# Optimization experiments

Hardware: AMD Instinct MI355X
Metric: run time of the kernel (lower is better)

Reference implementation:

```python
import jax, jax.numpy as jnp
import numpy as np

DIM = 1024
HEADS = 16
DIM_HEAD = 64
DEPTH = 12
LN_EPS = 1e-5


def setup_inputs() -> dict:
    key = jax.random.key(0)
    k1, k2, k3 = jax.random.split(key, 3)
    B, N = 4, 2048
    inner = HEADS * DIM_HEAD
    x = jax.random.normal(k1, (B, N, DIM), dtype=jnp.float32)
    ln_w = jnp.ones((DIM,), jnp.float32)
    ln_b = jnp.zeros((DIM,), jnp.float32)
    w_qkv = jax.random.normal(k2, (DIM, 3 * inner), jnp.float32) * (DIM ** -0.5)
    w_out = jax.random.normal(k3, (inner, DIM), jnp.float32) * (inner ** -0.5)
    b_out = jnp.zeros((DIM,), jnp.float32)
    return {"x": x, "ln_w": ln_w, "ln_b": ln_b, "w_qkv": w_qkv,
            "w_out": w_out, "b_out": b_out, "layer_index": 2}


def reference(x, ln_w, ln_b, w_qkv, w_out, b_out, layer_index):
    B, N, D = x.shape
    scale = DIM_HEAD ** -0.5
    # LayerNorm
    mu = jnp.mean(x, axis=-1, keepdims=True)
    var = jnp.mean(jnp.square(x - mu), axis=-1, keepdims=True)
    xn = (x - mu) * jax.lax.rsqrt(var + LN_EPS) * ln_w + ln_b
    # QKV projection (no bias), split heads: b n (h d) -> b h n d
    qkv = xn @ w_qkv  # [B, N, 3*H*Dh]
    q, k, v = jnp.split(qkv, 3, axis=-1)
    def heads(t):
        return t.reshape(B, N, HEADS, DIM_HEAD).transpose(0, 2, 1, 3)
    q, k, v = heads(q), heads(k), heads(v)
    dots = jnp.einsum('bhnd,bhmd->bhnm', q, k) * scale  # [B,H,N,N]
    if layer_index < DEPTH // 2:
        attn = jax.nn.relu(dots)
    else:
        attn = jax.nn.softmax(dots, axis=-1)
    attn = attn / N  # divide by x.shape[1]
    out = jnp.einsum('bhnm,bhmd->bhnd', attn, v)
    out = out.transpose(0, 2, 1, 3).reshape(B, N, HEADS * DIM_HEAD)
    # to_out (heads > 1): Linear + (inactive) dropout
    return out @ w_out + b_out
```

## Files before the change

### kernel.cpp

```cpp
#include <hip/hip_runtime.h>
#include <stdint.h>

typedef __bf16 bf16x8 __attribute__((ext_vector_type(8)));
typedef __bf16 bf16x4 __attribute__((ext_vector_type(4)));
typedef short short4s __attribute__((ext_vector_type(4)));
typedef float f32x4 __attribute__((ext_vector_type(4)));

#define PSCALE (0.125f / 2048.0f)

#define GLOAD16(src, dst)                                                      \
  __builtin_amdgcn_global_load_lds(                                            \
      (__attribute__((address_space(1))) void*)const_cast<__bf16*>(src),       \
      (__attribute__((address_space(3))) void*)(dst), 16, 0, 0)

__global__ __launch_bounds__(256) void ln_fused(const float* __restrict__ x,
                                                const float* __restrict__ w,
                                                const float* __restrict__ b,
                                                __bf16* __restrict__ xn) {
  const int row = blockIdx.x;
  const int t = threadIdx.x;
  const float4 v = ((const float4*)(x + (size_t)row * 1024))[t];
  float s = v.x + v.y + v.z + v.w;
  float ss = v.x * v.x + v.y * v.y + v.z * v.z + v.w * v.w;
#pragma unroll
  for (int o = 32; o; o >>= 1) {
    s += __shfl_down(s, o);
    ss += __shfl_down(ss, o);
  }
  __shared__ float red[8];
  if ((t & 63) == 0) {
    red[t >> 6] = s;
    red[4 + (t >> 6)] = ss;
  }
  __syncthreads();
  const float tot = red[0] + red[1] + red[2] + red[3];
  const float tot2 = red[4] + red[5] + red[6] + red[7];
  const float mu = tot * (1.0f / 1024.0f);
  const float var = tot2 * (1.0f / 1024.0f) - mu * mu;
  const float rs = rsqrtf(var + 1e-5f);
  const float4 wv = ((const float4*)w)[t];
  const float4 bv = ((const float4*)b)[t];
  bf16x4 o;
  o[0] = (__bf16)((v.x - mu) * rs * wv.x + bv.x);
  o[1] = (__bf16)((v.y - mu) * rs * wv.y + bv.y);
  o[2] = (__bf16)((v.z - mu) * rs * wv.z + bv.z);
  o[3] = (__bf16)((v.w - mu) * rs * wv.w + bv.w);
  ((bf16x4*)xn)[(size_t)row * 256 + t] = o;
}

__global__ __launch_bounds__(256) void transpose_cvt(const float* __restrict__ A,
                                                     __bf16* __restrict__ At,
                                                     int R, int C) {
  __shared__ __bf16 T[64][72];
  const int rb = blockIdx.y * 64, cb = blockIdx.x * 64;
  const int tid = threadIdx.x;
  const int r = tid >> 2, cg = tid & 3;
#pragma unroll
  for (int k = 0; k < 4; ++k) {
    const float4 v =
        *(const float4*)(A + (size_t)(rb + r) * C + cb + cg * 16 + k * 4);
    T[cg * 16 + k * 4 + 0][r] = (__bf16)v.x;
    T[cg * 16 + k * 4 + 1][r] = (__bf16)v.y;
    T[cg * 16 + k * 4 + 2][r] = (__bf16)v.z;
    T[cg * 16 + k * 4 + 3][r] = (__bf16)v.w;
  }
  __syncthreads();
#pragma unroll
  for (int i = 0; i < 2; ++i) {
    const int j = i * 256 + tid;
    const int c = j >> 3, s8 = j & 7;
    const bf16x8 o = *(const bf16x8*)&T[c][s8 * 8];
    *(bf16x8*)(At + (size_t)(cb + c) * R + rb + s8 * 8) = o;
  }
}

__device__ __forceinline__ void stage_128x64(const __bf16* __restrict__ g,
                                             int ld, __bf16* lds) {
  const int lane = threadIdx.x & 63, w = threadIdx.x >> 6;
#pragma unroll
  for (int i = 0; i < 4; ++i) {
    const int j = i * 256 + w * 64 + lane;
    const int row = j >> 3, slot = j & 7;
    const __bf16* src = g + (size_t)row * ld + ((slot ^ (row & 7)) << 3);
    GLOAD16(src, lds + (size_t)(i * 256 + w * 64) * 8);
  }
}

__device__ __forceinline__ void stage_vt(const __bf16* __restrict__ g,
                                         __bf16* lds) {
  const int lane = threadIdx.x & 63, w = threadIdx.x >> 6;
#pragma unroll
  for (int i = 0; i < 4; ++i) {
    const int j = i * 256 + w * 64 + lane;
    const int d = j >> 4, slot = j & 15;
    const __bf16* src = g + (size_t)d * 2048 + ((slot ^ (d & 7)) << 3);
    GLOAD16(src, lds + (size_t)(i * 256 + w * 64) * 8);
  }
}

template <int MODE>
__global__ __launch_bounds__(256) void gemm_nt(
    const __bf16* __restrict__ A, const __bf16* __restrict__ B, int K,
    float* __restrict__ outF, __bf16* __restrict__ Qo, __bf16* __restrict__ Ko,
    __bf16* __restrict__ Vto, const float* __restrict__ bias) {
  __shared__ __bf16 As[128 * 64];
  __shared__ __bf16 Bs[128 * 64];
  const int lane = threadIdx.x & 63, w = threadIdx.x >> 6;
  const int rb = blockIdx.y * 128, cb = blockIdx.x * 128;
  const int wr = (w >> 1) * 64, wc = (w & 1) * 64;
  f32x4 acc[4][4] = {};
  const __bf16* Ab = A + (size_t)rb * K;
  const __bf16* Bb = B + (size_t)cb * K;
  const int nkb = K >> 6;
  for (int kb = 0; kb < nkb; ++kb) {
    stage_128x64(Ab + kb * 64, K, As);
    stage_128x64(Bb + kb * 64, K, Bs);
    __syncthreads();
#pragma unroll
    for (int ks = 0; ks < 2; ++ks) {
      bf16x8 af[4], bfr[4];
      const int kc = ks * 4 + (lane >> 4);
#pragma unroll
      for (int rt = 0; rt < 4; ++rt) {
        const int lr = wr + rt * 16 + (lane & 15);
        af[rt] = *(const bf16x8*)(As + lr * 64 + ((kc ^ (lr & 7)) << 3));
      }
#pragma unroll
      for (int ct = 0; ct < 4; ++ct) {
        const int lc = wc + ct * 16 + (lane & 15);
        bfr[ct] = *(const bf16x8*)(Bs + lc * 64 + ((kc ^ (lc & 7)) << 3));
      }
#pragma unroll
      for (int rt = 0; rt < 4; ++rt)
#pragma unroll
        for (int ct = 0; ct < 4; ++ct)
          acc[rt][ct] = __builtin_amdgcn_mfma_f32_16x16x32_bf16(
              af[rt], bfr[ct], acc[rt][ct], 0, 0, 0);
    }
    __syncthreads();
  }
  const int r0 = rb + wr + (lane >> 4) * 4;
  if (MODE == 1) {
#pragma unroll
    for (int ct = 0; ct < 4; ++ct) {
      const int col = cb + wc + ct * 16 + (lane & 15);
      const float bv = bias[col];
#pragma unroll
      for (int rt = 0; rt < 4; ++rt) {
        const int row = r0 + rt * 16;
#pragma unroll
        for (int r = 0; r < 4; ++r)
          outF[(size_t)(row + r) * 1024 + col] = acc[rt][ct][r] + bv;
      }
    }
  } else {
#pragma unroll
    for (int ct = 0; ct < 4; ++ct) {
      const int col = cb + wc + ct * 16 + (lane & 15);
      const int part = col >> 10, rem = col & 1023;
      const int h = rem >> 6, d = rem & 63;
#pragma unroll
      for (int rt = 0; rt < 4; ++rt) {
        const int row = r0 + rt * 16;
        const int bi = row >> 11, n = row & 2047;
        const size_t bh = (size_t)bi * 16 + h;
        if (part == 2) {
          bf16x4 pv;
#pragma unroll
          for (int r = 0; r < 4; ++r) pv[r] = (__bf16)acc[rt][ct][r];
          *(bf16x4*)(Vto + (bh * 64 + d) * 2048 + n) = pv;
        } else if (part == 0) {
          __bf16* dst = Qo + (bh * 2048 + n) * 64 + d;
#pragma unroll
          for (int r = 0; r < 4; ++r)
            dst[(size_t)r * 64] = (__bf16)(acc[rt][ct][r] * PSCALE);
        } else {
          __bf16* dst = Ko + (bh * 2048 + n) * 64 + d;
#pragma unroll
          for (int r = 0; r < 4; ++r) dst[(size_t)r * 64] = (__bf16)acc[rt][ct][r];
        }
      }
    }
  }
}

__global__ __launch_bounds__(256, 4) void attn_relu(
    const __bf16* __restrict__ Q, const __bf16* __restrict__ K,
    const __bf16* __restrict__ Vt, __bf16* __restrict__ O) {
  __shared__ __bf16 Ks[128 * 64];
  __shared__ __bf16 Vs[64 * 128];
  const int lane = threadIdx.x & 63, w = threadIdx.x >> 6;
  const int g = lane >> 4, c15 = lane & 15;
  const int bh = blockIdx.y, qb = blockIdx.x;
  const __bf16* Qg = Q + ((size_t)bh * 2048 + qb * 128) * 64;
  const __bf16* Kg = K + (size_t)bh * 2048 * 64;
  const __bf16* Vg = Vt + (size_t)bh * 64 * 2048;

  bf16x8 qf[2][2];
#pragma unroll
  for (int rt = 0; rt < 2; ++rt)
#pragma unroll
    for (int ks = 0; ks < 2; ++ks) {
      const int row = w * 32 + rt * 16 + c15;
      qf[rt][ks] = *(const bf16x8*)(Qg + row * 64 + ks * 32 + (g << 3));
    }
  f32x4 oacc[2][4] = {};

  for (int kb = 0; kb < 16; ++kb) {
    stage_128x64(Kg + (size_t)kb * 128 * 64, 64, Ks);
    stage_vt(Vg + kb * 128, Vs);
    __syncthreads();
#pragma unroll
    for (int ct = 0; ct < 8; ++ct) {
      const int kr = ct * 16 + c15;
      const bf16x8 kf0 = *(const bf16x8*)(Ks + kr * 64 + ((g ^ (kr & 7)) << 3));
      const bf16x8 kf1 =
          *(const bf16x8*)(Ks + kr * 64 + (((4 + g) ^ (kr & 7)) << 3));
      f32x4 s0 = {}, s1 = {};
      s0 = __builtin_amdgcn_mfma_f32_16x16x32_bf16(kf0, qf[0][0], s0, 0, 0, 0);
      s0 = __builtin_amdgcn_mfma_f32_16x16x32_bf16(kf1, qf[0][1], s0, 0, 0, 0);
      s1 = __builtin_amdgcn_mfma_f32_16x16x32_bf16(kf0, qf[1][0], s1, 0, 0, 0);
      s1 = __builtin_amdgcn_mfma_f32_16x16x32_bf16(kf1, qf[1][1], s1, 0, 0, 0);
      bf16x4 p0, p1;
#pragma unroll
      for (int r = 0; r < 4; ++r) {
        p0[r] = (__bf16)fmaxf(s0[r], 0.0f);
        p1[r] = (__bf16)fmaxf(s1[r], 0.0f);
      }
      const short4s pa0 = __builtin_bit_cast(short4s, p0);
      const short4s pa1 = __builtin_bit_cast(short4s, p1);
      const int vchunk = 2 * ct + (g >> 1);
#pragma unroll
      for (int dt = 0; dt < 4; ++dt) {
        const int d = dt * 16 + c15;
        const bf16x4 vfr = *(const bf16x4*)(
            Vs + d * 128 + (((vchunk ^ (d & 7)) << 3) + 4 * (g & 1)));
        const short4s vb = __builtin_bit_cast(short4s, vfr);
        oacc[0][dt] = __builtin_amdgcn_mfma_f32_16x16x16bf16_1k(
            pa0, vb, oacc[0][dt], 0, 0, 0);
        oacc[1][dt] = __builtin_amdgcn_mfma_f32_16x16x16bf16_1k(
            pa1, vb, oacc[1][dt], 0, 0, 0);
      }
    }
    __syncthreads();
  }
  const int bi = bh >> 4, h = bh & 15;
#pragma unroll
  for (int rt = 0; rt < 2; ++rt)
#pragma unroll
    for (int dt = 0; dt < 4; ++dt) {
      const int col = h * 64 + dt * 16 + c15;
      const int n0 = qb * 128 + w * 32 + rt * 16 + g * 4;
      __bf16* dst = O + ((size_t)bi * 2048 + n0) * 1024 + col;
#pragma unroll
      for (int r = 0; r < 4; ++r) dst[(size_t)r * 1024] = (__bf16)oacc[rt][dt][r];
    }
}

extern "C" void kernel_launch(void* const* d_in, const int* in_sizes, int n_in,
                              void* d_out, int out_size, void* d_ws,
                              size_t ws_size, hipStream_t stream) {
  (void)in_sizes; (void)n_in; (void)out_size; (void)ws_size;
  const float* x = (const float*)d_in[0];
  const float* ln_w = (const float*)d_in[1];
  const float* ln_b = (const float*)d_in[2];
  const float* w_qkv = (const float*)d_in[3];
  const float* w_out = (const float*)d_in[4];
  const float* b_out = (const float*)d_in[5];
  char* ws = (char*)d_ws;
  __bf16* xn = (__bf16*)(ws);
  __bf16* Wt1 = (__bf16*)(ws + (size_t)(16u << 20));
  __bf16* Wt2 = (__bf16*)(ws + (size_t)(22u << 20));
  __bf16* Qb = (__bf16*)(ws + (size_t)(24u << 20));
  __bf16* Kb = (__bf16*)(ws + (size_t)(40u << 20));
  __bf16* Vtb = (__bf16*)(ws + (size_t)(56u << 20));
  __bf16* Ob = (__bf16*)(ws + (size_t)(72u << 20));
  float* out = (float*)d_out;

  ln_fused<<<8192, 256, 0, stream>>>(x, ln_w, ln_b, xn);
  transpose_cvt<<<dim3(48, 16), 256, 0, stream>>>(w_qkv, Wt1, 1024, 3072);
  transpose_cvt<<<dim3(16, 16), 256, 0, stream>>>(w_out, Wt2, 1024, 1024);
  gemm_nt<0><<<dim3(24, 64), 256, 0, stream>>>(xn, Wt1, 1024, nullptr, Qb, Kb,
                                               Vtb, nullptr);
  attn_relu<<<dim3(16, 64), 256, 0, stream>>>(Qb, Kb, Vtb, Ob);
  gemm_nt<1><<<dim3(8, 64), 256, 0, stream>>>(Ob, Wt2, 1024, out, nullptr,
                                              nullptr, nullptr, b_out);
}
```

Measured before the change: 188.5 us.

## Double-buffer K/V tiles and double query rows per block in relu attention

The relu attention kernel now loads the next K and V^T tiles into a second LDS buffer while computing on the current one, waiting with explicit vmcnt counts instead of a full sync before each tile. Each block handles 256 query rows (64 per wave), so every staged K/V tile is reused across twice as many queries. The grid is reordered so blocks of the same head are adjacent, and the V^T LDS swizzle is widened to 16 slots to cut bank conflicts. In exchange the kernel uses twice the LDS and more accumulator registers, drops the occupancy hint, and launches half as many blocks.

```diff
diff --git a/kernel.cpp b/kernel.cpp
--- a/kernel.cpp
+++ b/kernel.cpp
@@ -93,7 +93,7 @@
   for (int i = 0; i < 4; ++i) {
     const int j = i * 256 + w * 64 + lane;
     const int d = j >> 4, slot = j & 15;
-    const __bf16* src = g + (size_t)d * 2048 + ((slot ^ (d & 7)) << 3);
+    const __bf16* src = g + (size_t)d * 2048 + ((slot ^ (d & 15)) << 3);
     GLOAD16(src, lds + (size_t)(i * 256 + w * 64) * 8);
   }
 }
@@ -184,73 +184,87 @@
   }
 }
 
-__global__ __launch_bounds__(256, 4) void attn_relu(
+__global__ __launch_bounds__(256) void attn_relu(
     const __bf16* __restrict__ Q, const __bf16* __restrict__ K,
     const __bf16* __restrict__ Vt, __bf16* __restrict__ O) {
-  __shared__ __bf16 Ks[128 * 64];
-  __shared__ __bf16 Vs[64 * 128];
+  __shared__ __bf16 Ks[2][128 * 64];
+  __shared__ __bf16 Vs[2][64 * 128];
   const int lane = threadIdx.x & 63, w = threadIdx.x >> 6;
   const int g = lane >> 4, c15 = lane & 15;
-  const int bh = blockIdx.y, qb = blockIdx.x;
-  const __bf16* Qg = Q + ((size_t)bh * 2048 + qb * 128) * 64;
+  const int bh = blockIdx.x, qb = blockIdx.y;
+  const __bf16* Qg = Q + ((size_t)bh * 2048 + qb * 256) * 64;
   const __bf16* Kg = K + (size_t)bh * 2048 * 64;
   const __bf16* Vg = Vt + (size_t)bh * 64 * 2048;
 
-  bf16x8 qf[2][2];
-#pragma unroll
-  for (int rt = 0; rt < 2; ++rt)
+  bf16x8 qf[4][2];
+#pragma unroll
+  for (int rt = 0; rt < 4; ++rt)
 #pragma unroll
     for (int ks = 0; ks < 2; ++ks) {
-      const int row = w * 32 + rt * 16 + c15;
+      const int row = w * 64 + rt * 16 + c15;
       qf[rt][ks] = *(const bf16x8*)(Qg + row * 64 + ks * 32 + (g << 3));
     }
-  f32x4 oacc[2][4] = {};
+  f32x4 oacc[4][4] = {};
+
+  stage_128x64(Kg, 64, Ks[0]);
+  stage_vt(Vg, Vs[0]);
 
   for (int kb = 0; kb < 16; ++kb) {
-    stage_128x64(Kg + (size_t)kb * 128 * 64, 64, Ks);
-    stage_vt(Vg + kb * 128, Vs);
-    __syncthreads();
+    const int cur = kb & 1;
+    if (kb < 15) {
+      stage_128x64(Kg + (size_t)(kb + 1) * 128 * 64, 64, Ks[cur ^ 1]);
+      stage_vt(Vg + (kb + 1) * 128, Vs[cur ^ 1]);
+      asm volatile("s_waitcnt vmcnt(8)" ::: "memory");
+    } else {
+      asm volatile("s_waitcnt vmcnt(0)" ::: "memory");
+    }
+    __builtin_amdgcn_s_barrier();
+    const __bf16* __restrict__ Kc = Ks[cur];
+    const __bf16* __restrict__ Vc = Vs[cur];
 #pragma unroll
     for (int ct = 0; ct < 8; ++ct) {
       const int kr = ct * 16 + c15;
-      const bf16x8 kf0 = *(const bf16x8*)(Ks + kr * 64 + ((g ^ (kr & 7)) << 3));
+      const bf16x8 kf0 = *(const bf16x8*)(Kc + kr * 64 + ((g ^ (kr & 7)) << 3));
       const bf16x8 kf1 =
-          *(const bf16x8*)(Ks + kr * 64 + (((4 + g) ^ (kr & 7)) << 3));
-      f32x4 s0 = {}, s1 = {};
-      s0 = __builtin_amdgcn_mfma_f32_16x16x32_bf16(kf0, qf[0][0], s0, 0, 0, 0);
-      s0 = __builtin_amdgcn_mfma_f32_16x16x32_bf16(kf1, qf[0][1], s0, 0, 0, 0);
-      s1 = __builtin_amdgcn_mfma_f32_16x16x32_bf16(kf0, qf[1][0], s1, 0, 0, 0);
-      s1 = __builtin_amdgcn_mfma_f32_16x16x32_bf16(kf1, qf[1][1], s1, 0, 0, 0);
-      bf16x4 p0, p1;
-#pragma unroll
-      for (int r = 0; r < 4; ++r) {
-        p0[r] = (__bf16)fmaxf(s0[r], 0.0f);
-        p1[r] = (__bf16)fmaxf(s1[r], 0.0f);
-      }
-      const short4s pa0 = __builtin_bit_cast(short4s, p0);
-      const short4s pa1 = __builtin_bit_cast(short4s, p1);
+          *(const bf16x8*)(Kc + kr * 64 + (((4 + g) ^ (kr & 7)) << 3));
+      f32x4 s[4] = {{}, {}, {}, {}};
+#pragma unroll
+      for (int rt = 0; rt < 4; ++rt) {
+        s[rt] = __builtin_amdgcn_mfma_f32_16x16x32_bf16(kf0, qf[rt][0], s[rt],
+                                                        0, 0, 0);
+        s[rt] = __builtin_amdgcn_mfma_f32_16x16x32_bf16(kf1, qf[rt][1], s[rt],
+                                                        0, 0, 0);
+      }
+      short4s pa[4];
+#pragma unroll
+      for (int rt = 0; rt < 4; ++rt) {
+        bf16x4 p;
+#pragma unroll
+        for (int r = 0; r < 4; ++r) p[r] = (__bf16)fmaxf(s[rt][r], 0.0f);
+        pa[rt] = __builtin_bit_cast(short4s, p);
+      }
       const int vchunk = 2 * ct + (g >> 1);
 #pragma unroll
       for (int dt = 0; dt < 4; ++dt) {
         const int d = dt * 16 + c15;
         const bf16x4 vfr = *(const bf16x4*)(
-            Vs + d * 128 + (((vchunk ^ (d & 7)) << 3) + 4 * (g & 1)));
+            Vc + d * 128 + (((vchunk ^ c15) << 3) + 4 * (g & 1)));
         const short4s vb = __builtin_bit_cast(short4s, vfr);
-        oacc[0][dt] = __builtin_amdgcn_mfma_f32_16x16x16bf16_1k(
-            pa0, vb, oacc[0][dt], 0, 0, 0);
-        oacc[1][dt] = __builtin_amdgcn_mfma_f32_16x16x16bf16_1k(
-            pa1, vb, oacc[1][dt], 0, 0, 0);
-      }
-    }
-    __syncthreads();
+#pragma unroll
+        for (int rt = 0; rt < 4; ++rt)
+          oacc[rt][dt] = __builtin_amdgcn_mfma_f32_16x16x16bf16_1k(
+              pa[rt], vb, oacc[rt][dt], 0, 0, 0);
+      }
+    }
+    __builtin_amdgcn_s_barrier();
   }
   const int bi = bh >> 4, h = bh & 15;
 #pragma unroll
-  for (int rt = 0; rt < 2; ++rt)
+  for (int rt = 0; rt < 4; ++rt)
 #pragma unroll
     for (int dt = 0; dt < 4; ++dt) {
       const int col = h * 64 + dt * 16 + c15;
-      const int n0 = qb * 128 + w * 32 + rt * 16 + g * 4;
+      const int n0 = qb * 256 + w * 64 + rt * 16 + g * 4;
       __bf16* dst = O + ((size_t)bi * 2048 + n0) * 1024 + col;
 #pragma unroll
       for (int r = 0; r < 4; ++r) dst[(size_t)r * 1024] = (__bf16)oacc[rt][dt][r];
@@ -282,7 +296,7 @@
   transpose_cvt<<<dim3(16, 16), 256, 0, stream>>>(w_out, Wt2, 1024, 1024);
   gemm_nt<0><<<dim3(24, 64), 256, 0, stream>>>(xn, Wt1, 1024, nullptr, Qb, Kb,
                                                Vtb, nullptr);
-  attn_relu<<<dim3(16, 64), 256, 0, stream>>>(Qb, Kb, Vtb, Ob);
+  attn_relu<<<dim3(64, 8), 256, 0, stream>>>(Qb, Kb, Vtb, Ob);
   gemm_nt<1><<<dim3(8, 64), 256, 0, stream>>>(Ob, Wt2, 1024, out, nullptr,
                                               nullptr, nullptr, b_out);
 }
```

After: 189.8 us. About the same (+0.7%).
